# Optimization experiments

Hardware: AMD Instinct MI355X
Metric: run time of the kernel (lower is better)

## Reference

```python
import jax, jax.numpy as jnp
import numpy as np

N_COMPONENTS = 256
GAMMA = 1.0
TWO_PI = 6.283185307179586

def setup_inputs() -> dict:
    key = jax.random.key(0)
    k1, k2, k3, k4, k5 = jax.random.split(key, 5)
    B, D, OUT = 262144, 64, 18
    x = jax.random.normal(k1, (B, D), dtype=jnp.float32)
    # RBFSampler: random_weights_ = sqrt(2*gamma) * N(0,1), shape (D, n_components)
    W_rbf = jax.random.normal(k2, (D, N_COMPONENTS), dtype=jnp.float32)
    # random_offset_ = Uniform(0, 2*pi)
    b_rbf = jax.random.uniform(k3, (N_COMPONENTS,), dtype=jnp.float32)
    W_lin = jax.random.normal(k4, (OUT, N_COMPONENTS), dtype=jnp.float32) * (1.0 / np.sqrt(N_COMPONENTS))
    b_lin = jax.random.normal(k5, (OUT,), dtype=jnp.float32) * 0.01
    return {"x": x, "W_rbf": W_rbf, "b_rbf": b_rbf, "W_lin": W_lin, "b_lin": b_lin}

def reference(x, W_rbf, b_rbf, W_lin, b_lin):
    # RBF random-feature map (sklearn RBFSampler, gamma=1):
    # z = sqrt(2/n_components) * cos(x @ (sqrt(2*gamma)*W) + 2*pi*b)
    proj = x @ (jnp.sqrt(2.0 * GAMMA) * W_rbf) + TWO_PI * b_rbf  # [B, 256]
    feat = jnp.cos(proj) * jnp.sqrt(2.0 / N_COMPONENTS)          # [B, 256]
    # Linear head: feat @ W_lin.T + b_lin
    return feat @ W_lin.T + b_lin                                 # [B, 18]
```

## Files before the change

### kernel.cpp

```cpp
#include <hip/hip_runtime.h>
#include <cstdint>
#include <cstddef>

typedef __attribute__((ext_vector_type(8))) short bf16x8;
typedef __attribute__((ext_vector_type(8))) _Float16 f16x8;
typedef __attribute__((ext_vector_type(4))) float f32x4;
typedef __attribute__((ext_vector_type(2))) float f32x2;
typedef __attribute__((ext_vector_type(2))) unsigned int u32x2;

static constexpr int BROWS  = 262144;
static constexpr int DIM    = 64;
static constexpr int NC     = 256;
static constexpr int OUTD   = 18;
static constexpr int BM     = 32;
static constexpr int NCHTOT = BROWS / BM;
static constexpr int NBLK   = 768;

__device__ __forceinline__ unsigned cvt_pk_bf16(float a, float b) {
  unsigned r;
  asm("v_cvt_pk_bf16_f32 %0, %1, %2" : "=v"(r) : "v"(a), "v"(b));
  return r;
}

union U4 { unsigned u[4]; bf16x8 v; };

__device__ __forceinline__ bf16x8 pack8(const float* s) {
  U4 r;
#pragma unroll
  for (int p = 0; p < 4; ++p) r.u[p] = cvt_pk_bf16(s[2*p], s[2*p+1]);
  return r.v;
}

__global__ __launch_bounds__(512, 4) void rbf_fused(
    const float* __restrict__ x,  const float* __restrict__ Wr,
    const float* __restrict__ br, const float* __restrict__ Wl,
    const float* __restrict__ bl, float* __restrict__ out)
{
  __shared__ __align__(16) unsigned short xh16[2][BM * DIM];
  __shared__ __align__(16) unsigned short featb[2][BM * NC];

  const int tid  = threadIdx.x;
  const int wav  = tid >> 6;
  const int lane = tid & 63;
  const int li   = lane & 15;
  const int g    = lane >> 4;

  const float S1 = 0.22507907903927651f;
  const float SC = 0.08838834764831845f;

  f16x8 a1[2][2];
#pragma unroll
  for (int q = 0; q < 2; ++q) {
    const int n = 16 * (2*wav + q) + li;
#pragma unroll
    for (int kb = 0; kb < 2; ++kb) {
      f16x8 f;
#pragma unroll
      for (int j = 0; j < 8; ++j)
        f[j] = (_Float16)(Wr[(size_t)(32*kb + 8*g + j) * NC + n] * S1);
      a1[q][kb] = f;
    }
  }
  f32x4 brf[2];
#pragma unroll
  for (int q = 0; q < 2; ++q)
    brf[q] = *(const f32x4*)(br + 16*(2*wav + q) + 4*g);

  const f32x4 bl0 = *(const f32x4*)(bl + 4*g);
  const float bl16 = bl[16], bl17 = bl[17];
  const int rowc = (li < 2) ? (16 + li) : li;

  bf16x8 a2r[8] = {};
  if (wav < 4) {
    const int ot   = wav >> 1;
    const int arow = (ot == 0) ? li : rowc;
#pragma unroll
    for (int kb = 0; kb < 8; ++kb) {
      f32x4 v0 = *(const f32x4*)(Wl + arow*NC + 32*kb + 8*g);
      f32x4 v1 = *(const f32x4*)(Wl + arow*NC + 32*kb + 8*g + 4);
      float v[8];
      v[0]=v0.x; v[1]=v0.y; v[2]=v0.z; v[3]=v0.w;
      v[4]=v1.x; v[5]=v1.y; v[6]=v1.z; v[7]=v1.w;
      a2r[kb] = pack8(v);
    }
  }

  const int sr = tid >> 4;
  const int g4 = tid & 15;

  auto stage_write = [&](int p, f32x4 v) {
    union { _Float16 h[4]; u32x2 u; } cv;
    cv.h[0] = (_Float16)v.x; cv.h[1] = (_Float16)v.y;
    cv.h[2] = (_Float16)v.z; cv.h[3] = (_Float16)v.w;
    const int offs = sr*DIM + 8*((g4 >> 1) ^ (sr & 7)) + 4*(g4 & 1);
    *(u32x2*)(&xh16[p][offs]) = cv.u;
  };

  {
    const float* xp = x + ((size_t)blockIdx.x * BM + sr) * DIM + 4*g4;
    stage_write(0, *(const f32x4*)xp);
  }
  asm volatile("s_waitcnt lgkmcnt(0)" ::: "memory");
  __builtin_amdgcn_s_barrier();
  asm volatile("" ::: "memory");

  int pb = 0;
  for (int c = blockIdx.x; c < NCHTOT; c += NBLK, pb ^= 1) {
    const int R = c * BM;

    f32x4 pnext;
    const bool havenext = (c + NBLK < NCHTOT);
    if (havenext) {
      const float* xp = x + ((size_t)(c + NBLK) * BM + sr) * DIM + 4*g4;
      pnext = *(const f32x4*)xp;
    }

#pragma unroll
    for (int rt = 0; rt < 2; ++rt) {
      const int rr = rt*16 + li;
      const int m  = li & 7;
      f16x8 bh[2];
#pragma unroll
      for (int kb = 0; kb < 2; ++kb) {
        const int slot = 8*((4*kb + g) ^ m);
        bh[kb] = *(const f16x8*)(&xh16[pb][rr*DIM + slot]);
      }
      f32x4 acc[2];
#pragma unroll
      for (int q = 0; q < 2; ++q) acc[q] = f32x4{0.f, 0.f, 0.f, 0.f};
#pragma unroll
      for (int kb = 0; kb < 2; ++kb) {
#pragma unroll
        for (int q = 0; q < 2; ++q)
          acc[q] = __builtin_amdgcn_mfma_f32_16x16x32_f16(a1[q][kb], bh[kb], acc[q], 0, 0, 0);
      }
#pragma unroll
      for (int q = 0; q < 2; ++q) {
        float c4[4];
#pragma unroll
        for (int j = 0; j < 4; ++j) {
          float rev = acc[q][j] + brf[q][j];
          float f   = rev - floorf(rev);
          c4[j] = __builtin_amdgcn_cosf(f) * SC;
        }
        u32x2 pk;
        pk.x = cvt_pk_bf16(c4[0], c4[1]);
        pk.y = cvt_pk_bf16(c4[2], c4[3]);
        const int nt   = 2*wav + q;
        const int slot = (2*nt + (g >> 1)) ^ m;
        *(u32x2*)(&featb[pb][rr*256 + slot*8 + (g & 1)*4]) = pk;
      }
    }

    if (havenext) stage_write(pb ^ 1, pnext);

    asm volatile("s_waitcnt lgkmcnt(0)" ::: "memory");
    __builtin_amdgcn_s_barrier();
    asm volatile("" ::: "memory");

    if (wav < 4) {
      const int rt2 = wav & 1;
      const int ot  = wav >> 1;
      const int rr  = rt2*16 + li;
      const int m   = li & 7;
      f32x4 acc2 = f32x4{0.f,0.f,0.f,0.f};
#pragma unroll
      for (int kb = 0; kb < 8; ++kb) {
        bf16x8 b2 = *(const bf16x8*)(&featb[pb][rr*256 + (((4*kb + g) ^ m) * 8)]);
        acc2 = __builtin_amdgcn_mfma_f32_16x16x32_bf16(a2r[kb], b2, acc2, 0, 0, 0);
      }
      float* op = out + (size_t)(R + rr) * OUTD;
      if (ot == 0) {
        f32x2 s0; s0.x = acc2.x + bl0.x; s0.y = acc2.y + bl0.y;
        f32x2 s1; s1.x = acc2.z + bl0.z; s1.y = acc2.w + bl0.w;
        *(f32x2*)(op + 4*g)     = s0;
        *(f32x2*)(op + 4*g + 2) = s1;
      } else if (g == 0) {
        f32x2 s2; s2.x = acc2.x + bl16; s2.y = acc2.y + bl17;
        *(f32x2*)(op + 16) = s2;
      }
    }
  }
}

extern "C" void kernel_launch(void* const* d_in, const int* in_sizes, int n_in,
                              void* d_out, int out_size, void* d_ws, size_t ws_size,
                              hipStream_t stream) {
  (void)in_sizes; (void)n_in; (void)d_ws; (void)ws_size; (void)out_size;
  const float* x  = (const float*)d_in[0];
  const float* Wr = (const float*)d_in[1];
  const float* br = (const float*)d_in[2];
  const float* Wl = (const float*)d_in[3];
  const float* bl = (const float*)d_in[4];
  rbf_fused<<<NBLK, 512, 0, stream>>>(x, Wr, br, Wl, bl, (float*)d_out);
}
```

Measured before the change: 32.84 us.

## Double row tile to 64 so all eight waves run the output GEMM

Raises the rows per chunk from 32 to 64 and the grid from 768 to 512 blocks. Each thread now stages 8 floats of x with a 16-byte LDS write. With four 16-row tiles, all eight waves take part in the second MFMA stage (row tile × output tile) instead of only four. This gives more work per barrier and better wave use in the head GEMM. In exchange LDS doubles to about 72 KB per block, which may cut resident blocks per CU, and fewer chunks per block shortens the prefetch pipeline.

```diff
diff --git a/kernel.cpp b/kernel.cpp
--- a/kernel.cpp
+++ b/kernel.cpp
@@ -12,9 +12,9 @@
 static constexpr int DIM    = 64;
 static constexpr int NC     = 256;
 static constexpr int OUTD   = 18;
-static constexpr int BM     = 32;
+static constexpr int BM     = 64;
 static constexpr int NCHTOT = BROWS / BM;
-static constexpr int NBLK   = 768;
+static constexpr int NBLK   = 512;
 
 __device__ __forceinline__ unsigned cvt_pk_bf16(float a, float b) {
   unsigned r;
@@ -70,35 +70,36 @@
   const float bl16 = bl[16], bl17 = bl[17];
   const int rowc = (li < 2) ? (16 + li) : li;
 
-  bf16x8 a2r[8] = {};
-  if (wav < 4) {
-    const int ot   = wav >> 1;
-    const int arow = (ot == 0) ? li : rowc;
+  const int ot   = wav & 1;
+  const int rt2  = wav >> 1;
+  const int arow = (ot == 0) ? li : rowc;
+  bf16x8 a2r[8];
 #pragma unroll
-    for (int kb = 0; kb < 8; ++kb) {
-      f32x4 v0 = *(const f32x4*)(Wl + arow*NC + 32*kb + 8*g);
-      f32x4 v1 = *(const f32x4*)(Wl + arow*NC + 32*kb + 8*g + 4);
-      float v[8];
-      v[0]=v0.x; v[1]=v0.y; v[2]=v0.z; v[3]=v0.w;
-      v[4]=v1.x; v[5]=v1.y; v[6]=v1.z; v[7]=v1.w;
-      a2r[kb] = pack8(v);
-    }
+  for (int kb = 0; kb < 8; ++kb) {
+    f32x4 v0 = *(const f32x4*)(Wl + arow*NC + 32*kb + 8*g);
+    f32x4 v1 = *(const f32x4*)(Wl + arow*NC + 32*kb + 8*g + 4);
+    float v[8];
+    v[0]=v0.x; v[1]=v0.y; v[2]=v0.z; v[3]=v0.w;
+    v[4]=v1.x; v[5]=v1.y; v[6]=v1.z; v[7]=v1.w;
+    a2r[kb] = pack8(v);
   }
 
-  const int sr = tid >> 4;
-  const int g4 = tid & 15;
+  const int sr = tid >> 3;
+  const int sc = tid & 7;
 
-  auto stage_write = [&](int p, f32x4 v) {
-    union { _Float16 h[4]; u32x2 u; } cv;
-    cv.h[0] = (_Float16)v.x; cv.h[1] = (_Float16)v.y;
-    cv.h[2] = (_Float16)v.z; cv.h[3] = (_Float16)v.w;
-    const int offs = sr*DIM + 8*((g4 >> 1) ^ (sr & 7)) + 4*(g4 & 1);
-    *(u32x2*)(&xh16[p][offs]) = cv.u;
+  auto stage_write = [&](int p, f32x4 v0, f32x4 v1) {
+    union { _Float16 h[8]; U4 u4; } cv;
+    cv.h[0]=(_Float16)v0.x; cv.h[1]=(_Float16)v0.y;
+    cv.h[2]=(_Float16)v0.z; cv.h[3]=(_Float16)v0.w;
+    cv.h[4]=(_Float16)v1.x; cv.h[5]=(_Float16)v1.y;
+    cv.h[6]=(_Float16)v1.z; cv.h[7]=(_Float16)v1.w;
+    const int offs = sr*DIM + 8*(sc ^ (sr & 7));
+    *(bf16x8*)(&xh16[p][offs]) = cv.u4.v;
   };
 
   {
-    const float* xp = x + ((size_t)blockIdx.x * BM + sr) * DIM + 4*g4;
-    stage_write(0, *(const f32x4*)xp);
+    const float* xp = x + ((size_t)blockIdx.x * BM + sr) * DIM + 8*sc;
+    stage_write(0, *(const f32x4*)xp, *(const f32x4*)(xp + 4));
   }
   asm volatile("s_waitcnt lgkmcnt(0)" ::: "memory");
   __builtin_amdgcn_s_barrier();
@@ -108,15 +109,16 @@
   for (int c = blockIdx.x; c < NCHTOT; c += NBLK, pb ^= 1) {
     const int R = c * BM;
 
-    f32x4 pnext;
+    f32x4 pn0, pn1;
     const bool havenext = (c + NBLK < NCHTOT);
     if (havenext) {
-      const float* xp = x + ((size_t)(c + NBLK) * BM + sr) * DIM + 4*g4;
-      pnext = *(const f32x4*)xp;
+      const float* xp = x + ((size_t)(c + NBLK) * BM + sr) * DIM + 8*sc;
+      pn0 = *(const f32x4*)xp;
+      pn1 = *(const f32x4*)(xp + 4);
     }
 
 #pragma unroll
-    for (int rt = 0; rt < 2; ++rt) {
+    for (int rt = 0; rt < 4; ++rt) {
       const int rr = rt*16 + li;
       const int m  = li & 7;
       f16x8 bh[2];
@@ -152,17 +154,15 @@
       }
     }
 
-    if (havenext) stage_write(pb ^ 1, pnext);
+    if (havenext) stage_write(pb ^ 1, pn0, pn1);
 
     asm volatile("s_waitcnt lgkmcnt(0)" ::: "memory");
     __builtin_amdgcn_s_barrier();
     asm volatile("" ::: "memory");
 
-    if (wav < 4) {
-      const int rt2 = wav & 1;
-      const int ot  = wav >> 1;
-      const int rr  = rt2*16 + li;
-      const int m   = li & 7;
+    {
+      const int rr = rt2*16 + li;
+      const int m  = li & 7;
       f32x4 acc2 = f32x4{0.f,0.f,0.f,0.f};
 #pragma unroll
       for (int kb = 0; kb < 8; ++kb) {
```

After: 36.12 us. 10.0% more time.
